# Performance work log

Measured on AMD Instinct MI355X. Metric: run time of the kernel, lower is better.

Reference implementation:

```python
import jax, jax.numpy as jnp
import numpy as np

B, S, D, H, FF = 2, 2048, 1024, 16, 4096
DK = D // H
EPS = 1e-5


def setup_inputs() -> dict:
    key = jax.random.key(0)
    ks = jax.random.split(key, 16)
    sd = 0.02
    return {
        "x": jax.random.normal(ks[0], (B, S, D), jnp.float32),
        "mask": jnp.ones((B, 1, 1, S), jnp.int32),
        "wq_w": jax.random.normal(ks[1], (D, D), jnp.float32) * sd,
        "wq_b": jnp.zeros((D,), jnp.float32),
        "wk_w": jax.random.normal(ks[2], (D, D), jnp.float32) * sd,
        "wk_b": jnp.zeros((D,), jnp.float32),
        "wv_w": jax.random.normal(ks[3], (D, D), jnp.float32) * sd,
        "wv_b": jnp.zeros((D,), jnp.float32),
        "wo_w": jax.random.normal(ks[4], (D, D), jnp.float32) * sd,
        "wo_b": jnp.zeros((D,), jnp.float32),
        "ff1_w": jax.random.normal(ks[5], (FF, D), jnp.float32) * sd,
        "ff1_b": jnp.zeros((FF,), jnp.float32),
        "ff2_w": jax.random.normal(ks[6], (D, FF), jnp.float32) * sd,
        "ff2_b": jnp.zeros((D,), jnp.float32),
        "ln1_a": jnp.ones((D,), jnp.float32),
        "ln1_b": jnp.zeros((D,), jnp.float32),
        "ln2_a": jnp.ones((D,), jnp.float32),
        "ln2_b": jnp.zeros((D,), jnp.float32),
    }


def _layernorm(x, alpha, beta):
    # Matches torch module: std is unbiased (ddof=1), divides by (std + eps)
    mean = jnp.mean(x, -1, keepdims=True)
    std = jnp.std(x, -1, keepdims=True, ddof=1)
    return (x - mean) / (std + EPS) * alpha + beta


def _mha(x, mask, wq_w, wq_b, wk_w, wk_b, wv_w, wv_b, wo_w, wo_b):
    q = (x @ wq_w.T + wq_b).reshape(B, S, H, DK).transpose(0, 2, 1, 3)
    k = (x @ wk_w.T + wk_b).reshape(B, S, H, DK).transpose(0, 2, 1, 3)
    v = (x @ wv_w.T + wv_b).reshape(B, S, H, DK).transpose(0, 2, 1, 3)
    scores = jnp.einsum('bhqd,bhkd->bhqk', q, k) / jnp.sqrt(jnp.float32(DK))
    scores = jnp.where(mask == 0, -jnp.inf, scores)
    attn = jax.nn.softmax(scores, axis=-1)
    out = jnp.einsum('bhqk,bhkd->bhqd', attn, v)
    out = out.transpose(0, 2, 1, 3).reshape(B, S, D)
    return out @ wo_w.T + wo_b


def reference(x, mask, wq_w, wq_b, wk_w, wk_b, wv_w, wv_b, wo_w, wo_b,
              ff1_w, ff1_b, ff2_w, ff2_b, ln1_a, ln1_b, ln2_a, ln2_b):
    # Residual 1: pre-norm + self-attention (dropout = 0)
    h = _layernorm(x, ln1_a, ln1_b)
    x = x + _mha(h, mask, wq_w, wq_b, wk_w, wk_b, wv_w, wv_b, wo_w, wo_b)
    # Residual 2: pre-norm + FFN
    h = _layernorm(x, ln2_a, ln2_b)
    ff = jax.nn.relu(h @ ff1_w.T + ff1_b) @ ff2_w.T + ff2_b
    return x + ff
```

## Files before the change

### kernel.cpp

```cpp
#include <hip/hip_runtime.h>
#include <hip/hip_bf16.h>
#include <stdint.h>

#define B_   2
#define S_   2048
#define D_   1024
#define H_   16
#define FF_  4096
#define TOK  4096
#define EPS_ 1e-5f
#define SC2  0.18033688f

typedef __attribute__((ext_vector_type(8))) short short8;
typedef __attribute__((ext_vector_type(4))) short short4_t;
typedef __attribute__((ext_vector_type(4))) float float4_t;

__device__ __forceinline__ short f2bf(float f) {
  union { float f; uint32_t u; } v; v.f = f;
  uint32_t r = v.u + 0x7fffu + ((v.u >> 16) & 1u);
  return (short)(r >> 16);
}

__device__ __forceinline__ uint32_t pkbf(float a, float b) {
  __hip_bfloat162 h = __float22bfloat162_rn(make_float2(a, b));
  union { __hip_bfloat162 h; uint32_t u; } c; c.h = h; return c.u;
}

__device__ __forceinline__ void gload_lds16(const void* g, void* l) {
  __builtin_amdgcn_global_load_lds(
      (const __attribute__((address_space(1))) void*)g,
      (__attribute__((address_space(3))) void*)l, 16, 0, 0);
}

__global__ void cvt_all(const float* __restrict__ wq, const float* __restrict__ wk,
                        const float* __restrict__ wv, const float* __restrict__ wo,
                        const float* __restrict__ f1, const float* __restrict__ f2,
                        short* __restrict__ out) {
  const int n4 = (12 << 20) / 4;
  int idx = blockIdx.x * blockDim.x + threadIdx.x;
  int stride = gridDim.x * blockDim.x;
  for (int j4 = idx; j4 < n4; j4 += stride) {
    const int j = j4 * 4;
    const int seg = j >> 20;
    const float* src; int off;
    if (seg < 4)      { src = (seg == 0) ? wq : (seg == 1) ? wk : (seg == 2) ? wv : wo;
                        off = j & ((1 << 20) - 1); }
    else if (seg < 8) { src = f1; off = j - (4 << 20); }
    else              { src = f2; off = j - (8 << 20); }
    float4_t v = *(const float4_t*)(src + off);
    short4_t o = { f2bf(v[0]), f2bf(v[1]), f2bf(v[2]), f2bf(v[3]) };
    *(short4_t*)(out + j) = o;
  }
}

__global__ void mask_kernel(const int* __restrict__ m, float* __restrict__ o,
                            int* __restrict__ flags) {
  const int i = blockIdx.x * 64 + threadIdx.x;
  const int mv = m[i];
  o[i] = mv ? 0.0f : -1e30f;
  unsigned long long bal = __ballot(mv == 0);
  if (threadIdx.x == 0) flags[blockIdx.x] = (bal != 0ull) ? 1 : 0;
}

__global__ void combine_kernel(const float* __restrict__ x2, const float* __restrict__ p0,
                               float* __restrict__ out, const float* __restrict__ bias, int n) {
  int idx = blockIdx.x * blockDim.x + threadIdx.x;
  int stride = gridDim.x * blockDim.x;
  for (int j = idx * 4; j < n; j += stride * 4) {
    float4_t a = *(const float4_t*)(x2 + j);
    float4_t b = *(const float4_t*)(p0 + j);
    float4_t c = *(const float4_t*)(out + j);
    float4_t bb = *(const float4_t*)(bias + (j & (D_ - 1)));
    float4_t o = { a[0]+b[0]+c[0]+bb[0], a[1]+b[1]+c[1]+bb[1],
                   a[2]+b[2]+c[2]+bb[2], a[3]+b[3]+c[3]+bb[3] };
    *(float4_t*)(out + j) = o;
  }
}

__global__ __launch_bounds__(256) void ln_kernel(
    const float* __restrict__ x, const float* __restrict__ alpha,
    const float* __restrict__ beta, short* __restrict__ out)
{
  const int row = blockIdx.x;
  const int tid = threadIdx.x;
  const float4_t v = *(const float4_t*)(x + (size_t)row * D_ + tid * 4);
  float s  = v[0] + v[1] + v[2] + v[3];
  float ss = v[0]*v[0] + v[1]*v[1] + v[2]*v[2] + v[3]*v[3];
  #pragma unroll
  for (int m = 1; m < 64; m <<= 1) { s += __shfl_xor(s, m); ss += __shfl_xor(ss, m); }
  __shared__ float red[8];
  const int wave = tid >> 6, lane = tid & 63;
  if (lane == 0) { red[wave] = s; red[4 + wave] = ss; }
  __syncthreads();
  s  = red[0] + red[1] + red[2] + red[3];
  ss = red[4] + red[5] + red[6] + red[7];
  const float mean = s * (1.0f / D_);
  float var = (ss - (float)D_ * mean * mean) * (1.0f / (D_ - 1));
  var = fmaxf(var, 0.0f);
  const float inv = 1.0f / (sqrtf(var) + EPS_);
  short4_t o;
  #pragma unroll
  for (int j = 0; j < 4; j++) {
    float a = alpha[tid*4 + j], bb = beta[tid*4 + j];
    o[j] = f2bf((v[j] - mean) * inv * a + bb);
  }
  *(short4_t*)(out + (size_t)row * D_ + tid * 4) = o;
}

template<int EPI, int BN>
__global__ __launch_bounds__(256) void gemm_bt(
    const short* __restrict__ A, const short* __restrict__ Bm,
    void* __restrict__ Cout, void* __restrict__ Cout2,
    const float* __restrict__ bias, const float* __restrict__ res,
    int N, int K, int lda, int ldb)
{
  __shared__ __align__(16) short As[2][128][32];
  __shared__ __align__(16) short Bs[2][BN][32];

  const int tid  = threadIdx.x;
  const int wave = tid >> 6, lane = tid & 63;
  const int l15  = lane & 15, l4 = lane >> 4;

  const int gx = gridDim.x, gy = gridDim.y;
  int bid = (blockIdx.z * gy + blockIdx.y) * gx + blockIdx.x;
  const int q8 = (gx * gy * gridDim.z) >> 3;
  bid = (bid & 7) * q8 + (bid >> 3);
  const int n0 = (bid % gx) * BN;
  const int m0 = ((bid / gx) % gy) * 128;
  const int zi = bid / (gx * gy);
  const int koff = zi * K;

  constexpr int MI = (BN == 128) ? 4 : 2;
  const int rb = (BN == 128) ? (wave >> 1) * 64 : wave * 32;
  const int cb = (BN == 128) ? (wave & 1) * 64 : 0;

  float4_t acc[MI][4] = {};

  const int scol = (lane & 3) * 8;
  const short* gA0 = A + (size_t)(m0 + wave*32 + (lane >> 2)) * lda + koff + scol;
  const short* gA1 = gA0 + (size_t)16 * lda;
  const short* gB0;
  const short* gB1 = nullptr;
  if (BN == 128) {
    gB0 = Bm + (size_t)(n0 + wave*32 + (lane >> 2)) * ldb + koff + scol;
    gB1 = gB0 + (size_t)16 * ldb;
  } else {
    gB0 = Bm + (size_t)(n0 + wave*16 + (lane >> 2)) * ldb + koff + scol;
  }

  gload_lds16(gA0, &As[0][wave*32][0]);
  gload_lds16(gA1, &As[0][wave*32 + 16][0]);
  if (BN == 128) {
    gload_lds16(gB0, &Bs[0][wave*32][0]);
    gload_lds16(gB1, &Bs[0][wave*32 + 16][0]);
  } else {
    gload_lds16(gB0, &Bs[0][wave*16][0]);
  }

  for (int k0 = 0; k0 < K; k0 += 32) {
    const int cur = (k0 >> 5) & 1;
    __syncthreads();
    if (k0 + 32 < K) {
      gload_lds16(gA0 + k0 + 32, &As[cur^1][wave*32][0]);
      gload_lds16(gA1 + k0 + 32, &As[cur^1][wave*32 + 16][0]);
      if (BN == 128) {
        gload_lds16(gB0 + k0 + 32, &Bs[cur^1][wave*32][0]);
        gload_lds16(gB1 + k0 + 32, &Bs[cur^1][wave*32 + 16][0]);
      } else {
        gload_lds16(gB0 + k0 + 32, &Bs[cur^1][wave*16][0]);
      }
    }
    short8 af[MI], bf[4];
    #pragma unroll
    for (int i = 0; i < MI; i++)
      af[i] = *(const short8*)&As[cur][rb + i*16 + l15][l4*8];
    #pragma unroll
    for (int i = 0; i < 4; i++)
      bf[i] = *(const short8*)&Bs[cur][cb + i*16 + l15][l4*8];
    #pragma unroll
    for (int mi = 0; mi < MI; mi++)
      #pragma unroll
      for (int ni = 0; ni < 4; ni++)
        acc[mi][ni] = __builtin_amdgcn_mfma_f32_16x16x32_bf16(af[mi], bf[ni], acc[mi][ni], 0, 0, 0);
  }

  const int crow0 = m0 + rb + l4*4;
  const int ccol0 = n0 + cb + l15;
  float* dstf = (float*)((EPI == 4 && zi == 1) ? Cout2 : Cout);
  #pragma unroll
  for (int mi = 0; mi < MI; mi++) {
    #pragma unroll
    for (int ni = 0; ni < 4; ni++) {
      const int col = ccol0 + ni*16;
      const float bc = (EPI == 4) ? 0.0f : bias[col];
      #pragma unroll
      for (int r = 0; r < 4; r++) {
        const int row = crow0 + mi*16 + r;
        const float v = acc[mi][ni][r];
        if (EPI == 2) {
          ((short*)Cout)[(size_t)row * N + col] = f2bf(fmaxf(v + bc, 0.0f));
        } else if (EPI == 3) {
          ((float*)Cout)[(size_t)row * N + col] =
              res[(size_t)row * N + col] + v + bc;
        } else {
          dstf[(size_t)row * N + col] = v;
        }
      }
    }
  }
}

__global__ __launch_bounds__(256) void qkv_gemm(
    const short* __restrict__ A, const short* __restrict__ Bm,
    short* __restrict__ qkbuf, short* __restrict__ vt,
    const float* __restrict__ qb, const float* __restrict__ kb,
    const float* __restrict__ vb)
{
  __shared__ __align__(16) short As[2][128][32];
  __shared__ __align__(16) short Bs[2][128][32];

  const int tid  = threadIdx.x;
  const int wave = tid >> 6, lane = tid & 63;
  const int l15  = lane & 15, l4 = lane >> 4;

  const int gx = gridDim.x;
  int bid = blockIdx.y * gx + blockIdx.x;
  const int q8 = (gx * gridDim.y) >> 3;
  bid = (bid & 7) * q8 + (bid >> 3);
  const int n0 = (bid % gx) * 128;
  const int m0 = (bid / gx) * 128;

  const int rb = (wave >> 1) * 64;
  const int cb = (wave & 1) * 64;

  float4_t acc[4][4] = {};

  const int scol = (lane & 3) * 8;
  const short* gA0 = A  + (size_t)(m0 + wave*32 + (lane >> 2)) * 1024 + scol;
  const short* gA1 = gA0 + (size_t)16 * 1024;
  const short* gB0 = Bm + (size_t)(n0 + wave*32 + (lane >> 2)) * 1024 + scol;
  const short* gB1 = gB0 + (size_t)16 * 1024;

  gload_lds16(gA0, &As[0][wave*32][0]);
  gload_lds16(gA1, &As[0][wave*32 + 16][0]);
  gload_lds16(gB0, &Bs[0][wave*32][0]);
  gload_lds16(gB1, &Bs[0][wave*32 + 16][0]);

  for (int k0 = 0; k0 < 1024; k0 += 32) {
    const int cur = (k0 >> 5) & 1;
    __syncthreads();
    if (k0 + 32 < 1024) {
      gload_lds16(gA0 + k0 + 32, &As[cur^1][wave*32][0]);
      gload_lds16(gA1 + k0 + 32, &As[cur^1][wave*32 + 16][0]);
      gload_lds16(gB0 + k0 + 32, &Bs[cur^1][wave*32][0]);
      gload_lds16(gB1 + k0 + 32, &Bs[cur^1][wave*32 + 16][0]);
    }
    short8 af[4], bf[4];
    #pragma unroll
    for (int i = 0; i < 4; i++)
      af[i] = *(const short8*)&As[cur][rb + i*16 + l15][l4*8];
    #pragma unroll
    for (int i = 0; i < 4; i++)
      bf[i] = *(const short8*)&Bs[cur][cb + i*16 + l15][l4*8];
    #pragma unroll
    for (int mi = 0; mi < 4; mi++)
      #pragma unroll
      for (int ni = 0; ni < 4; ni++)
        acc[mi][ni] = __builtin_amdgcn_mfma_f32_16x16x32_bf16(af[mi], bf[ni], acc[mi][ni], 0, 0, 0);
  }

  const int crow0 = m0 + rb + l4*4;
  const int ccol0 = n0 + cb + l15;
  const int seg = n0 >> 10;
  if (seg < 2) {
    const float* bb = seg ? kb : qb;
    const float scl = seg ? 1.0f : SC2;
    #pragma unroll
    for (int mi = 0; mi < 4; mi++)
      #pragma unroll
      for (int ni = 0; ni < 4; ni++) {
        const int col = ccol0 + ni*16;
        const float bc = bb[col & 1023];
        #pragma unroll
        for (int r = 0; r < 4; r++)
          qkbuf[(size_t)(crow0 + mi*16 + r) * 2048 + col] =
              f2bf((acc[mi][ni][r] + bc) * scl);
      }
  } else {
    #pragma unroll
    for (int mi = 0; mi < 4; mi++)
      #pragma unroll
      for (int ni = 0; ni < 4; ni++) {
        const int d = ccol0 + ni*16 - 2048;
        const float bc = vb[d];
        short4_t o = { f2bf(acc[mi][ni][0] + bc), f2bf(acc[mi][ni][1] + bc),
                       f2bf(acc[mi][ni][2] + bc), f2bf(acc[mi][ni][3] + bc) };
        *(short4_t*)&vt[(size_t)d * TOK + crow0 + mi*16] = o;
      }
  }
}

__global__ __launch_bounds__(256, 4) void attn_kernel(
    const short* __restrict__ qk, const short* __restrict__ vt,
    const float* __restrict__ maskb, const int* __restrict__ mflags,
    short* __restrict__ out)
{
  int bid = (blockIdx.z * H_ + blockIdx.y) * (S_/64) + blockIdx.x;
  bid = (bid & 7) * ((B_ * H_ * (S_/64)) >> 3) + (bid >> 3);
  const int qt = bid % (S_/64);
  const int h  = (bid / (S_/64)) % H_;
  const int b  = bid / ((S_/64) * H_);

  const int tid = threadIdx.x, wave = tid >> 6, lane = tid & 63;
  const int l15 = lane & 15, l4 = lane >> 4;
  const int q0 = qt * 64 + wave * 16;

  __shared__ __align__(16) short Kt[2][4096];
  __shared__ __align__(16) short Vt[2][4096];

  short8 qa[2];
  #pragma unroll
  for (int kc = 0; kc < 2; kc++)
    qa[kc] = *(const short8*)&qk[(size_t)(b*S_ + q0 + l15) * 2048 + h*64 + kc*32 + l4*8];

  short8 ones;
  #pragma unroll
  for (int i = 0; i < 8; i++) ones[i] = (short)0x3F80;

  float4_t acc[4];
  #pragma unroll
  for (int dg = 0; dg < 4; dg++) acc[dg] = (float4_t){0.f, 0.f, 0.f, 0.f};
  float4_t accl = (float4_t){0.f, 0.f, 0.f, 0.f};
  float m2 = 0.0f;

  const int r8 = lane >> 3;
  const int ch = (lane & 7) ^ ((r8 & 3) | ((wave & 1) << 2));
  const int sbase = wave * 512;

  #pragma unroll
  for (int i = 0; i < 2; i++) {
    const int row = i*32 + wave*8 + r8;
    gload_lds16(qk + (size_t)(b*S_ + row) * 2048 + 1024 + h*64 + ch*8, &Kt[0][sbase + i*2048]);
    gload_lds16(vt + (size_t)(h*64 + row) * TOK + b*S_ + ch*8,         &Vt[0][sbase + i*2048]);
  }

  int krow[4];
  #pragma unroll
  for (int kg = 0; kg < 4; kg++)
    krow[kg] = 32*(kg>>1) + 8*(l15>>2) + 4*(kg&1) + (l15&3);
  const int gq = (l15 & 3) | (((l15 >> 2) & 1) << 2);
  const int gv = (l15 & 3) | (((l15 >> 3) & 1) << 2);

  for (int t = 0; t < S_/64; t++) {
    const int cur = t & 1;
    __syncthreads();
    if (t + 1 < S_/64) {
      const int k1 = (t + 1) * 64;
      #pragma unroll
      for (int i = 0; i < 2; i++) {
        const int row = i*32 + wave*8 + r8;
        gload_lds16(qk + (size_t)(b*S_ + k1 + row) * 2048 + 1024 + h*64 + ch*8, &Kt[cur^1][sbase + i*2048]);
        gload_lds16(vt + (size_t)(h*64 + row) * TOK + b*S_ + k1 + ch*8,         &Vt[cur^1][sbase + i*2048]);
      }
    }
    const short* Kc = &Kt[cur][0];
    const short* Vc = &Vt[cur][0];

    short8 kf[4][2], vf[4][2];
    #pragma unroll
    for (int kg = 0; kg < 4; kg++)
      #pragma unroll
      for (int kc = 0; kc < 2; kc++)
        kf[kg][kc] = *(const short8*)(Kc + krow[kg]*64 + ((l4 + kc*4) ^ gq) * 8);
    #pragma unroll
    for (int dg = 0; dg < 4; dg++)
      #pragma unroll
      for (int pc = 0; pc < 2; pc++)
        vf[dg][pc] = *(const short8*)(Vc + (dg*16 + l15)*64 + ((l4 + pc*4) ^ gv) * 8);

    const float negm2 = -m2;
    float4_t sc[4];
    #pragma unroll
    for (int kg = 0; kg < 4; kg++)
      sc[kg] = (float4_t){negm2, negm2, negm2, negm2};
    __builtin_amdgcn_s_setprio(1);
    #pragma unroll
    for (int kg = 0; kg < 4; kg++)
      #pragma unroll
      for (int kc = 0; kc < 2; kc++)
        sc[kg] = __builtin_amdgcn_mfma_f32_16x16x32_bf16(kf[kg][kc], qa[kc], sc[kg], 0, 0, 0);
    __builtin_amdgcn_s_setprio(0);

    if (mflags[b*(S_/64) + t]) {
      #pragma unroll
      for (int kg = 0; kg < 4; kg++) {
        float4_t mb = *(const float4_t*)&maskb[b*S_ + t*64 + 32*(kg>>1) + 4*(kg&1) + 8*l4];
        #pragma unroll
        for (int r = 0; r < 4; r++) sc[kg][r] += mb[r];
      }
    }

    float pm = fmaxf(fmaxf(sc[0][0], sc[0][1]), sc[0][2]);
    pm = fmaxf(fmaxf(pm, sc[0][3]), sc[1][0]);
    pm = fmaxf(fmaxf(pm, sc[1][1]), sc[1][2]);
    pm = fmaxf(fmaxf(pm, sc[1][3]), sc[2][0]);
    pm = fmaxf(fmaxf(pm, sc[2][1]), sc[2][2]);
    pm = fmaxf(fmaxf(pm, sc[2][3]), sc[3][0]);
    pm = fmaxf(fmaxf(pm, sc[3][1]), sc[3][2]);
    pm = fmaxf(pm, sc[3][3]);
    pm = fmaxf(pm, __shfl_xor(pm, 16));
    pm = fmaxf(pm, __shfl_xor(pm, 32));
    if (__any(pm > 8.0f)) {
      const float shift = fmaxf(pm, 0.0f);
      m2 += shift;
      const float esc = exp2f(-shift);
      #pragma unroll
      for (int r = 0; r < 4; r++) {
        const float er = __shfl(esc, l4*4 + r);
        #pragma unroll
        for (int dg = 0; dg < 4; dg++) acc[dg][r] *= er;
        accl[r] *= er;
      }
      #pragma unroll
      for (int kg = 0; kg < 4; kg++)
        #pragma unroll
        for (int r = 0; r < 4; r++) sc[kg][r] -= shift;
    }
    #pragma unroll
    for (int kg = 0; kg < 4; kg++)
      #pragma unroll
      for (int r = 0; r < 4; r++)
        sc[kg][r] = exp2f(sc[kg][r]);

    union { short8 s8; uint32_t u[4]; } pu[2];
    #pragma unroll
    for (int pc = 0; pc < 2; pc++) {
      pu[pc].u[0] = pkbf(sc[2*pc][0],   sc[2*pc][1]);
      pu[pc].u[1] = pkbf(sc[2*pc][2],   sc[2*pc][3]);
      pu[pc].u[2] = pkbf(sc[2*pc+1][0], sc[2*pc+1][1]);
      pu[pc].u[3] = pkbf(sc[2*pc+1][2], sc[2*pc+1][3]);
    }
    __builtin_amdgcn_s_setprio(1);
    #pragma unroll
    for (int dg = 0; dg < 4; dg++)
      #pragma unroll
      for (int pc = 0; pc < 2; pc++)
        acc[dg] = __builtin_amdgcn_mfma_f32_16x16x32_bf16(pu[pc].s8, vf[dg][pc], acc[dg], 0, 0, 0);
    #pragma unroll
    for (int pc = 0; pc < 2; pc++)
      accl = __builtin_amdgcn_mfma_f32_16x16x32_bf16(pu[pc].s8, ones, accl, 0, 0, 0);
    __builtin_amdgcn_s_setprio(0);
  }

  float linv[4];
  #pragma unroll
  for (int r = 0; r < 4; r++) linv[r] = 1.0f / accl[r];
  #pragma unroll
  for (int dg = 0; dg < 4; dg++)
    #pragma unroll
    for (int r = 0; r < 4; r++)
      out[(size_t)(b*S_ + q0 + l4*4 + r) * D_ + h*64 + dg*16 + l15] =
          f2bf(acc[dg][r] * linv[r]);
}

extern "C" void kernel_launch(void* const* d_in, const int* in_sizes, int n_in,
                              void* d_out, int out_size, void* d_ws, size_t ws_size,
                              hipStream_t stream)
{
  const float* x     = (const float*)d_in[0];
  const int*   mask  = (const int*)d_in[1];
  const float* wq_w  = (const float*)d_in[2];
  const float* wq_b  = (const float*)d_in[3];
  const float* wk_w  = (const float*)d_in[4];
  const float* wk_b  = (const float*)d_in[5];
  const float* wv_w  = (const float*)d_in[6];
  const float* wv_b  = (const float*)d_in[7];
  const float* wo_w  = (const float*)d_in[8];
  const float* wo_b  = (const float*)d_in[9];
  const float* ff1_w = (const float*)d_in[10];
  const float* ff1_b = (const float*)d_in[11];
  const float* ff2_w = (const float*)d_in[12];
  const float* ff2_b = (const float*)d_in[13];
  const float* ln1_a = (const float*)d_in[14];
  const float* ln1_b = (const float*)d_in[15];
  const float* ln2_a = (const float*)d_in[16];
  const float* ln2_b = (const float*)d_in[17];

  uint8_t* ws = (uint8_t*)d_ws;
  const size_t MB = 1024 * 1024;
  short* wqkv  = (short*)(ws + 0);
  short* wob   = (short*)(ws + 6*MB);
  short* ff1b  = (short*)(ws + 8*MB);
  short* ff2b  = (short*)(ws + 16*MB);
  float* maskb = (float*)(ws + 24*MB + 64*1024);
  int*   mflg  = (int*)(ws + 24*MB + 128*1024);
  short* h1    = (short*)(ws + 25*MB);
  short* attno = (short*)(ws + 25*MB);
  short* qkbuf = (short*)(ws + 33*MB);
  short* vt    = (short*)(ws + 49*MB);
  float* x2    = (float*)(ws + 65*MB);
  short* ffa   = (short*)(ws + 33*MB);
  float* p0f   = (float*)(ws + 0);

  cvt_all<<<2048, 256, 0, stream>>>(wq_w, wk_w, wv_w, wo_w, ff1_w, ff2_w, (short*)ws);
  mask_kernel<<<TOK/64, 64, 0, stream>>>(mask, maskb, mflg);
  ln_kernel<<<TOK, 256, 0, stream>>>(x, ln1_a, ln1_b, h1);
  qkv_gemm<<<dim3(3072/128, TOK/128), 256, 0, stream>>>(
      h1, wqkv, qkbuf, vt, wq_b, wk_b, wv_b);
  attn_kernel<<<dim3(S_/64, H_, B_), 256, 0, stream>>>(qkbuf, vt, maskb, mflg, attno);
  gemm_bt<3,64><<<dim3(1024/64, TOK/128), 256, 0, stream>>>(
      attno, wob, x2, nullptr, wo_b, x, 1024, 1024, 1024, 1024);
  ln_kernel<<<TOK, 256, 0, stream>>>(x2, ln2_a, ln2_b, h1);
  gemm_bt<2,128><<<dim3(FF_/128, TOK/128), 256, 0, stream>>>(
      h1, ff1b, ffa, nullptr, ff1_b, nullptr, FF_, 1024, 1024, 1024);
  gemm_bt<4,128><<<dim3(1024/128, TOK/128, 2), 256, 0, stream>>>(
      ffa, ff2b, p0f, d_out, nullptr, nullptr, 1024, 2048, FF_, FF_);
  combine_kernel<<<2048, 256, 0, stream>>>(x2, p0f, (float*)d_out, ff2_b, TOK * D_);
}
```

Before: 285.2 us.

## Replace QKV and FF1 GEMMs with 256x256-tile 8-wave pipelined kernels

Adds a shared 256x256-tile GEMM main loop using 512 threads, K-steps of 64, a swizzled LDS layout and double buffering with explicit vmcnt waits. MFMA phases are interleaved with LDS reads and staging, and wave priority is raised around the MFMA phases. The QKV projection and FF1+ReLU now use this loop in place of 128x128-tile kernels, to raise operand reuse and reduce global and LDS traffic per flop. The larger tiles give fewer blocks (192 for QKV), which may leave CUs idle, and each block uses 128 KB of LDS, which limits occupancy.

```diff
diff --git a/kernel.cpp b/kernel.cpp
--- a/kernel.cpp
+++ b/kernel.cpp
@@ -197,9 +197,7 @@
       for (int r = 0; r < 4; r++) {
         const int row = crow0 + mi*16 + r;
         const float v = acc[mi][ni][r];
-        if (EPI == 2) {
-          ((short*)Cout)[(size_t)row * N + col] = f2bf(fmaxf(v + bc, 0.0f));
-        } else if (EPI == 3) {
+        if (EPI == 3) {
           ((float*)Cout)[(size_t)row * N + col] =
               res[(size_t)row * N + col] + v + bc;
         } else {
@@ -210,92 +208,166 @@
   }
 }
 
-__global__ __launch_bounds__(256) void qkv_gemm(
+#define G256_DECLS                                                            \
+  const int tid = threadIdx.x;                                                \
+  const int w = tid >> 6, lane = tid & 63;                                    \
+  const int wm = w >> 2, wn = w & 3;                                          \
+  const int l15 = lane & 15, l4 = lane >> 4;                                  \
+  const int srow = w*8 + (lane >> 3);                                         \
+  const int schk = ((lane & 7) ^ (((lane >> 5) & 1) << 1)) * 8;               \
+  const int rswz = (l4 ^ (((l15 >> 2) & 1) << 1)) * 8;                        \
+  const int aoff = (wm*128 + l15) * 64 + rswz;                                \
+  const int boff = (wn*64  + l15) * 64 + rswz;
+
+#define G256_STG(buf_, koff_) do {                                            \
+    short* da = lds + (buf_)*16384 + w*512;                                   \
+    short* db = lds + 32768 + (buf_)*16384 + w*512;                           \
+    const short* sa = gA + (koff_);                                           \
+    const short* sb = gB + (koff_);                                           \
+    gload_lds16(sa,             da);                                          \
+    gload_lds16(sa +  64*1024,  da + 4096);                                   \
+    gload_lds16(sa + 128*1024,  da + 8192);                                   \
+    gload_lds16(sa + 192*1024,  da + 12288);                                  \
+    gload_lds16(sb,             db);                                          \
+    gload_lds16(sb +  64*1024,  db + 4096);                                   \
+    gload_lds16(sb + 128*1024,  db + 8192);                                   \
+    gload_lds16(sb + 192*1024,  db + 12288);                                  \
+  } while (0)
+
+#define G256_LOOP                                                             \
+  float4_t acc[8][4] = {};                                                    \
+  G256_STG(0, 0);                                                             \
+  G256_STG(1, 64);                                                            \
+  for (int t = 0; t < 16; ++t) {                                              \
+    const int cur = t & 1;                                                    \
+    if (t < 15) asm volatile("s_waitcnt vmcnt(8)" ::: "memory");              \
+    else        asm volatile("s_waitcnt vmcnt(0)" ::: "memory");              \
+    __builtin_amdgcn_s_barrier();                                             \
+    __builtin_amdgcn_sched_barrier(0);                                        \
+    const short* La = lds + cur*16384 + aoff;                                 \
+    const short* Lb = lds + 32768 + cur*16384 + boff;                         \
+    short8 af[4][2], bf0[2][2], bf1[2][2];                                    \
+    _Pragma("unroll") for (int mf = 0; mf < 4; mf++)                          \
+      _Pragma("unroll") for (int ks = 0; ks < 2; ks++)                        \
+        af[mf][ks] = *(const short8*)(La + mf*1024 + ks*32);                  \
+    _Pragma("unroll") for (int nf = 0; nf < 2; nf++)                          \
+      _Pragma("unroll") for (int ks = 0; ks < 2; ks++)                        \
+        bf0[nf][ks] = *(const short8*)(Lb + nf*1024 + ks*32);                 \
+    _Pragma("unroll") for (int nf = 0; nf < 2; nf++)                          \
+      _Pragma("unroll") for (int ks = 0; ks < 2; ks++)                        \
+        bf1[nf][ks] = *(const short8*)(Lb + (2+nf)*1024 + ks*32);             \
+    __builtin_amdgcn_s_setprio(1);                                            \
+    _Pragma("unroll") for (int mf = 0; mf < 4; mf++)                          \
+      _Pragma("unroll") for (int nf = 0; nf < 2; nf++)                        \
+        _Pragma("unroll") for (int ks = 0; ks < 2; ks++)                      \
+          acc[mf][nf] = __builtin_amdgcn_mfma_f32_16x16x32_bf16(              \
+              af[mf][ks], bf0[nf][ks], acc[mf][nf], 0, 0, 0);                 \
+    __builtin_amdgcn_s_setprio(0);                                            \
+    short8 a2[4][2];                                                          \
+    _Pragma("unroll") for (int mf = 0; mf < 4; mf++)                          \
+      _Pragma("unroll") for (int ks = 0; ks < 2; ks++)                        \
+        a2[mf][ks] = *(const short8*)(La + (4+mf)*1024 + ks*32);              \
+    __builtin_amdgcn_s_setprio(1);                                            \
+    _Pragma("unroll") for (int mf = 0; mf < 4; mf++)                          \
+      _Pragma("unroll") for (int nf = 0; nf < 2; nf++)                        \
+        _Pragma("unroll") for (int ks = 0; ks < 2; ks++)                      \
+          acc[mf][2+nf] = __builtin_amdgcn_mfma_f32_16x16x32_bf16(            \
+              af[mf][ks], bf1[nf][ks], acc[mf][2+nf], 0, 0, 0);               \
+    _Pragma("unroll") for (int mf = 0; mf < 4; mf++)                          \
+      _Pragma("unroll") for (int nf = 0; nf < 2; nf++)                        \
+        _Pragma("unroll") for (int ks = 0; ks < 2; ks++)                      \
+          acc[4+mf][2+nf] = __builtin_amdgcn_mfma_f32_16x16x32_bf16(          \
+              a2[mf][ks], bf1[nf][ks], acc[4+mf][2+nf], 0, 0, 0);             \
+    __builtin_amdgcn_s_setprio(0);                                            \
+    __builtin_amdgcn_s_barrier();        \
+    if (t < 14) G256_STG(cur, (t+2)*64);                                      \
+    __builtin_amdgcn_s_setprio(1);                                            \
+    _Pragma("unroll") for (int mf = 0; mf < 4; mf++)                          \
+      _Pragma("unroll") for (int nf = 0; nf < 2; nf++)                        \
+        _Pragma("unroll") for (int ks = 0; ks < 2; ks++)                      \
+          acc[4+mf][nf] = __builtin_amdgcn_mfma_f32_16x16x32_bf16(            \
+              a2[mf][ks], bf0[nf][ks], acc[4+mf][nf], 0, 0, 0);               \
+    __builtin_amdgcn_s_setprio(0);                                            \
+  }
+
+__global__ __launch_bounds__(512, 2) void ff1_256(
+    const short* __restrict__ A, const short* __restrict__ Bm,
+    short* __restrict__ Cout, const float* __restrict__ bias)
+{
+  __shared__ __align__(16) short lds[65536];
+  G256_DECLS
+  const int gx = gridDim.x;
+  int bid = blockIdx.y * gx + blockIdx.x;
+  const int q8 = (gx * gridDim.y) >> 3;
+  bid = (bid & 7) * q8 + (bid >> 3);
+  const int n0 = (bid % gx) * 256;
+  const int m0 = (bid / gx) * 256;
+  const short* gA = A  + (size_t)(m0 + srow) * 1024 + schk;
+  const short* gB = Bm + (size_t)(n0 + srow) * 1024 + schk;
+
+  G256_LOOP
+
+  #pragma unroll
+  for (int mf = 0; mf < 8; mf++) {
+    #pragma unroll
+    for (int nf = 0; nf < 4; nf++) {
+      const int col = n0 + wn*64 + nf*16 + l15;
+      const float bc = bias[col];
+      #pragma unroll
+      for (int r = 0; r < 4; r++) {
+        const int row = m0 + wm*128 + mf*16 + l4*4 + r;
+        Cout[(size_t)row * FF_ + col] = f2bf(fmaxf(acc[mf][nf][r] + bc, 0.0f));
+      }
+    }
+  }
+}
+
+__global__ __launch_bounds__(512, 2) void qkv_256(
     const short* __restrict__ A, const short* __restrict__ Bm,
     short* __restrict__ qkbuf, short* __restrict__ vt,
     const float* __restrict__ qb, const float* __restrict__ kb,
     const float* __restrict__ vb)
 {
-  __shared__ __align__(16) short As[2][128][32];
-  __shared__ __align__(16) short Bs[2][128][32];
-
-  const int tid  = threadIdx.x;
-  const int wave = tid >> 6, lane = tid & 63;
-  const int l15  = lane & 15, l4 = lane >> 4;
-
+  __shared__ __align__(16) short lds[65536];
+  G256_DECLS
   const int gx = gridDim.x;
   int bid = blockIdx.y * gx + blockIdx.x;
   const int q8 = (gx * gridDim.y) >> 3;
   bid = (bid & 7) * q8 + (bid >> 3);
-  const int n0 = (bid % gx) * 128;
-  const int m0 = (bid / gx) * 128;
-
-  const int rb = (wave >> 1) * 64;
-  const int cb = (wave & 1) * 64;
-
-  float4_t acc[4][4] = {};
-
-  const int scol = (lane & 3) * 8;
-  const short* gA0 = A  + (size_t)(m0 + wave*32 + (lane >> 2)) * 1024 + scol;
-  const short* gA1 = gA0 + (size_t)16 * 1024;
-  const short* gB0 = Bm + (size_t)(n0 + wave*32 + (lane >> 2)) * 1024 + scol;
-  const short* gB1 = gB0 + (size_t)16 * 1024;
-
-  gload_lds16(gA0, &As[0][wave*32][0]);
-  gload_lds16(gA1, &As[0][wave*32 + 16][0]);
-  gload_lds16(gB0, &Bs[0][wave*32][0]);
-  gload_lds16(gB1, &Bs[0][wave*32 + 16][0]);
-
-  for (int k0 = 0; k0 < 1024; k0 += 32) {
-    const int cur = (k0 >> 5) & 1;
-    __syncthreads();
-    if (k0 + 32 < 1024) {
-      gload_lds16(gA0 + k0 + 32, &As[cur^1][wave*32][0]);
-      gload_lds16(gA1 + k0 + 32, &As[cur^1][wave*32 + 16][0]);
-      gload_lds16(gB0 + k0 + 32, &Bs[cur^1][wave*32][0]);
-      gload_lds16(gB1 + k0 + 32, &Bs[cur^1][wave*32 + 16][0]);
-    }
-    short8 af[4], bf[4];
-    #pragma unroll
-    for (int i = 0; i < 4; i++)
-      af[i] = *(const short8*)&As[cur][rb + i*16 + l15][l4*8];
-    #pragma unroll
-    for (int i = 0; i < 4; i++)
-      bf[i] = *(const short8*)&Bs[cur][cb + i*16 + l15][l4*8];
-    #pragma unroll
-    for (int mi = 0; mi < 4; mi++)
-      #pragma unroll
-      for (int ni = 0; ni < 4; ni++)
-        acc[mi][ni] = __builtin_amdgcn_mfma_f32_16x16x32_bf16(af[mi], bf[ni], acc[mi][ni], 0, 0, 0);
-  }
-
-  const int crow0 = m0 + rb + l4*4;
-  const int ccol0 = n0 + cb + l15;
+  const int n0 = (bid % gx) * 256;
+  const int m0 = (bid / gx) * 256;
+  const short* gA = A  + (size_t)(m0 + srow) * 1024 + schk;
+  const short* gB = Bm + (size_t)(n0 + srow) * 1024 + schk;
+
+  G256_LOOP
+
   const int seg = n0 >> 10;
   if (seg < 2) {
     const float* bb = seg ? kb : qb;
     const float scl = seg ? 1.0f : SC2;
     #pragma unroll
-    for (int mi = 0; mi < 4; mi++)
-      #pragma unroll
-      for (int ni = 0; ni < 4; ni++) {
-        const int col = ccol0 + ni*16;
+    for (int mf = 0; mf < 8; mf++)
+      #pragma unroll
+      for (int nf = 0; nf < 4; nf++) {
+        const int col = n0 + wn*64 + nf*16 + l15;
         const float bc = bb[col & 1023];
         #pragma unroll
-        for (int r = 0; r < 4; r++)
-          qkbuf[(size_t)(crow0 + mi*16 + r) * 2048 + col] =
-              f2bf((acc[mi][ni][r] + bc) * scl);
+        for (int r = 0; r < 4; r++) {
+          const int row = m0 + wm*128 + mf*16 + l4*4 + r;
+          qkbuf[(size_t)row * 2048 + col] = f2bf((acc[mf][nf][r] + bc) * scl);
+        }
       }
   } else {
     #pragma unroll
-    for (int mi = 0; mi < 4; mi++)
-      #pragma unroll
-      for (int ni = 0; ni < 4; ni++) {
-        const int d = ccol0 + ni*16 - 2048;
+    for (int mf = 0; mf < 8; mf++)
+      #pragma unroll
+      for (int nf = 0; nf < 4; nf++) {
+        const int d = n0 + wn*64 + nf*16 + l15 - 2048;
         const float bc = vb[d];
-        short4_t o = { f2bf(acc[mi][ni][0] + bc), f2bf(acc[mi][ni][1] + bc),
-                       f2bf(acc[mi][ni][2] + bc), f2bf(acc[mi][ni][3] + bc) };
-        *(short4_t*)&vt[(size_t)d * TOK + crow0 + mi*16] = o;
+        const int row0 = m0 + wm*128 + mf*16 + l4*4;
+        short4_t o = { f2bf(acc[mf][nf][0] + bc), f2bf(acc[mf][nf][1] + bc),
+                       f2bf(acc[mf][nf][2] + bc), f2bf(acc[mf][nf][3] + bc) };
+        *(short4_t*)&vt[(size_t)d * TOK + row0] = o;
       }
   }
 }
@@ -505,14 +577,13 @@
   cvt_all<<<2048, 256, 0, stream>>>(wq_w, wk_w, wv_w, wo_w, ff1_w, ff2_w, (short*)ws);
   mask_kernel<<<TOK/64, 64, 0, stream>>>(mask, maskb, mflg);
   ln_kernel<<<TOK, 256, 0, stream>>>(x, ln1_a, ln1_b, h1);
-  qkv_gemm<<<dim3(3072/128, TOK/128), 256, 0, stream>>>(
+  qkv_256<<<dim3(3072/256, TOK/256), 512, 0, stream>>>(
       h1, wqkv, qkbuf, vt, wq_b, wk_b, wv_b);
   attn_kernel<<<dim3(S_/64, H_, B_), 256, 0, stream>>>(qkbuf, vt, maskb, mflg, attno);
   gemm_bt<3,64><<<dim3(1024/64, TOK/128), 256, 0, stream>>>(
       attno, wob, x2, nullptr, wo_b, x, 1024, 1024, 1024, 1024);
   ln_kernel<<<TOK, 256, 0, stream>>>(x2, ln2_a, ln2_b, h1);
-  gemm_bt<2,128><<<dim3(FF_/128, TOK/128), 256, 0, stream>>>(
-      h1, ff1b, ffa, nullptr, ff1_b, nullptr, FF_, 1024, 1024, 1024);
+  ff1_256<<<dim3(FF_/256, TOK/256), 512, 0, stream>>>(h1, ff1b, ffa, ff1_b);
   gemm_bt<4,128><<<dim3(1024/128, TOK/128, 2), 256, 0, stream>>>(
       ffa, ff2b, p0f, d_out, nullptr, nullptr, 1024, 2048, FF_, FF_);
   combine_kernel<<<2048, 256, 0, stream>>>(x2, p0f, (float*)d_out, ff2_b, TOK * D_);
```

Measured after the change: 250.6 us. 12.1% less time.
